# Kernel optimization log

Hardware: AMD Instinct MI355X
Metric: run time of the kernel (lower is better)

## Reference

```python
import jax, jax.numpy as jnp
import numpy as np

N_NODES = 100000
N_EDGES = 1600000
D_FEAT = 64  # node feature dim; apply_func indim = 2*D_FEAT, outdim = D_FEAT


def setup_inputs() -> dict:
    key = jax.random.key(0)
    k1, k2, k3, k4 = jax.random.split(key, 4)
    h = jax.random.normal(k1, (N_NODES, D_FEAT), dtype=jnp.float32)
    src = jax.random.randint(k2, (N_EDGES,), 0, N_NODES, dtype=jnp.int32)
    dst = jax.random.randint(k3, (N_EDGES,), 0, N_NODES, dtype=jnp.int32)
    W = jax.random.normal(k4, (D_FEAT, 2 * D_FEAT), dtype=jnp.float32) / jnp.sqrt(2.0 * D_FEAT)
    b = jnp.zeros((D_FEAT,), dtype=jnp.float32)
    return {"h": h, "W": W, "b": b, "src": src, "dst": dst}


def reference(h, W, b, src, dst):
    n = h.shape[0]
    # message passing: gather source features, mean-reduce per destination node
    msgs = h[src]                                                # [E, D]
    summed = jax.ops.segment_sum(msgs, dst, num_segments=n)     # [N, D]
    deg = jax.ops.segment_sum(jnp.ones(dst.shape, h.dtype), dst, num_segments=n)  # [N]
    c = summed / jnp.maximum(deg, 1.0)[:, None]                 # mean aggregate
    # update: concat(h, c) -> linear -> L2 normalize -> relu
    bundle = jnp.concatenate([h, c], axis=1) @ W.T + b           # [N, D]
    norm = jnp.linalg.norm(bundle, axis=1, keepdims=True)
    bundle = bundle / jnp.maximum(norm, 1e-12)                   # F.normalize(p=2, dim=1)
    new_h = jax.nn.relu(bundle)
    # DGL update_all only touches nodes that received messages
    h_upd = jnp.where(deg[:, None] > 0, new_h, h)
    # residual (indim == outdim)
    return h + h_upd
```

## Files before the change

kernel.cpp:

```cpp
#include <hip/hip_runtime.h>

#define DF 64
#define ELLK 32
#define NB 512
#define BSTR 3584
#define NPB 196
#define NSL 4

typedef __attribute__((ext_vector_type(8))) short bf16x8;
typedef __attribute__((ext_vector_type(4))) float f32x4;

__device__ __forceinline__ unsigned short bf16rne(float f) {
    unsigned u = __float_as_uint(f);
    unsigned r = u + 0x7fffu + ((u >> 16) & 1u);
    return (unsigned short)(r >> 16);
}
__device__ __forceinline__ float b2f(unsigned short u) {
    return __uint_as_float((unsigned)u << 16);
}

__global__ __launch_bounds__(256) void conv_zero(
    const float* __restrict__ h, unsigned short* __restrict__ hbs,
    int* __restrict__ gcur, int* __restrict__ ovfcnt, int N)
{
    int tid = blockIdx.x * 256 + threadIdx.x;
    if (tid < NB) gcur[tid] = 0;
    if (tid == NB) *ovfcnt = 0;
    if (tid < N * 8) {
        int n = tid >> 3, s8 = tid & 7;
        const float* hp = &h[(size_t)n * DF + s8 * 8];
        float4 v0 = *(const float4*)hp;
        float4 v1 = *(const float4*)(hp + 4);
        ushort4 o0, o1;
        o0.x = bf16rne(v0.x); o0.y = bf16rne(v0.y); o0.z = bf16rne(v0.z); o0.w = bf16rne(v0.w);
        o1.x = bf16rne(v1.x); o1.y = bf16rne(v1.y); o1.z = bf16rne(v1.z); o1.w = bf16rne(v1.w);
        unsigned short* op = &hbs[((size_t)(s8 >> 1) * (N + 1) + n) * 16 + (s8 & 1) * 8];
        *(ushort4*)op = o0;
        *(ushort4*)(op + 4) = o1;
    }
}

#define EPT 13
__global__ __launch_bounds__(256) void bin_edges(
    const int* __restrict__ src, const int* __restrict__ dst,
    int* __restrict__ gcur, unsigned* __restrict__ pairs,
    int* __restrict__ ovf, int* __restrict__ ovfcnt, int ovfcap, int E, int N)
{
    __shared__ unsigned hist[NB];
    __shared__ unsigned base_s[NB];
    int t = threadIdx.x;
    for (int i = t; i < NB; i += 256) hist[i] = 0;
    __syncthreads();

    int e0 = blockIdx.x * (EPT * 256);
    unsigned pk[EPT];
    #pragma unroll
    for (int k = 0; k < EPT; ++k) {
        int e = e0 + k * 256 + t;
        pk[k] = 0xFFFFFFFFu;
        if (e < E) {
            int d = dst[e];
            unsigned bkt = (unsigned)(((unsigned long long)d * NB) / (unsigned)N);
            unsigned r = atomicAdd(&hist[bkt], 1u);
            pk[k] = (r << 9) | bkt;
        }
    }
    __syncthreads();
    int rot = (blockIdx.x * 67) & (NB - 1);
    for (int i = t; i < NB; i += 256) {
        int ii = (i + rot) & (NB - 1);
        unsigned hv = hist[ii];
        if (hv) base_s[ii] = (unsigned)atomicAdd(&gcur[ii], (int)hv);
    }
    __syncthreads();

    #pragma unroll
    for (int k = 0; k < EPT; ++k) {
        if (pk[k] != 0xFFFFFFFFu) {
            int e = e0 + k * 256 + t;
            int d = dst[e], s = src[e];
            unsigned bkt = pk[k] & (NB - 1u);
            unsigned pos = base_s[bkt] + (pk[k] >> 9);
            if (pos < BSTR) {
                int lo = (int)(((long long)bkt * N + NB - 1) / NB);
                pairs[(size_t)bkt * BSTR + pos] = ((unsigned)(d - lo) << 17) | (unsigned)s;
            } else {
                int p = atomicAdd(ovfcnt, 1);
                if (p < ovfcap) { ovf[2 * p] = d; ovf[2 * p + 1] = s; }
            }
        }
    }
}

__global__ __launch_bounds__(256) void build_ell(
    const unsigned* __restrict__ pairs, const int* __restrict__ gcur,
    int* __restrict__ cnt, int* __restrict__ ell,
    int* __restrict__ ovf, int* __restrict__ ovfcnt, int ovfcap, int N)
{
    __shared__ int ell_l[NPB * ELLK];
    __shared__ int cnt_l[NPB];
    int b = blockIdx.x, t = threadIdx.x;
    int lo = (int)(((long long)b * N + NB - 1) / NB);
    int hi = (int)(((long long)(b + 1) * N + NB - 1) / NB);
    if (hi > N) hi = N;
    int nn = hi - lo;
    for (int i = t; i < nn; i += 256) cnt_l[i] = 0;
    __syncthreads();

    int count = gcur[b]; if (count > BSTR) count = BSTR;
    const unsigned* pb = &pairs[(size_t)b * BSTR];
    for (int i = t; i < count; i += 256) {
        unsigned p = pb[i];
        int ld = (int)(p >> 17);
        int s  = (int)(p & 131071u);
        int slot = atomicAdd(&cnt_l[ld], 1);
        if (slot < ELLK) {
            ell_l[ld * ELLK + (((slot & 7) << 2) | (slot >> 3))] = s;
        } else {
            int q = atomicAdd(ovfcnt, 1);
            if (q < ovfcap) { ovf[2 * q] = lo + ld; ovf[2 * q + 1] = s; }
        }
    }
    __syncthreads();

    int total = nn * ELLK;
    int* eout = &ell[(size_t)lo * ELLK];
    for (int i = t; i < total; i += 256) eout[i] = ell_l[i];
    for (int i = t; i < nn; i += 256) {
        int c = cnt_l[i];
        cnt[lo + i] = c < ELLK ? c : ELLK;
    }
}

__global__ __launch_bounds__(512) void gather_slice(
    const unsigned short* __restrict__ hbs, const int* __restrict__ cnt,
    const int* __restrict__ ell, unsigned short* __restrict__ csum, int N)
{
    int slice = blockIdx.x & 3;
    int wave = threadIdx.x >> 6, lane = threadIdx.x & 63;
    const int ns = lane >> 4;
    const int q  = lane & 15;
    const int nb = q >> 1;
    const int fp = q & 1;
    const unsigned short* tab = hbs + (size_t)slice * (N + 1) * 16;
    unsigned short* cs = csum + (size_t)slice * N * 16;

    int gw = (blockIdx.x >> 2) * 8 + wave;
    int nw = (gridDim.x >> 2) * 8;

    for (int n0 = gw * 4; n0 < N; n0 += nw * 4) {
        int n = n0 + ns;
        bool valid = (n < N);
        int m = valid ? cnt[n] : 0;
        const int* erow = &ell[(size_t)(valid ? n : 0) * ELLK];
        int4 pv = *(const int4*)(erow + nb * 4);

        bf16x8 v0 = {0,0,0,0,0,0,0,0};
        bf16x8 v1 = {0,0,0,0,0,0,0,0};
        bf16x8 v2 = {0,0,0,0,0,0,0,0};
        bf16x8 v3 = {0,0,0,0,0,0,0,0};
        if (nb      < m) v0 = *(const bf16x8*)&tab[(size_t)pv.x * 16 + fp * 8];
        if (nb +  8 < m) v1 = *(const bf16x8*)&tab[(size_t)pv.y * 16 + fp * 8];
        if (nb + 16 < m) v2 = *(const bf16x8*)&tab[(size_t)pv.z * 16 + fp * 8];
        if (nb + 24 < m) v3 = *(const bf16x8*)&tab[(size_t)pv.w * 16 + fp * 8];

        f32x4 lo, hi;
        #pragma unroll
        for (int i = 0; i < 4; ++i) {
            lo[i] = (b2f((unsigned short)v0[i])     + b2f((unsigned short)v1[i]))
                  + (b2f((unsigned short)v2[i])     + b2f((unsigned short)v3[i]));
            hi[i] = (b2f((unsigned short)v0[4 + i]) + b2f((unsigned short)v1[4 + i]))
                  + (b2f((unsigned short)v2[4 + i]) + b2f((unsigned short)v3[4 + i]));
        }

        #pragma unroll
        for (int msk = 2; msk <= 8; msk <<= 1) {
            #pragma unroll
            for (int i = 0; i < 4; ++i) {
                lo[i] += __shfl_xor(lo[i], msk);
                hi[i] += __shfl_xor(hi[i], msk);
            }
        }

        if (valid && nb == 0) {
            bf16x8 o;
            o[0] = (short)bf16rne(lo[0]); o[1] = (short)bf16rne(lo[1]);
            o[2] = (short)bf16rne(lo[2]); o[3] = (short)bf16rne(lo[3]);
            o[4] = (short)bf16rne(hi[0]); o[5] = (short)bf16rne(hi[1]);
            o[6] = (short)bf16rne(hi[2]); o[7] = (short)bf16rne(hi[3]);
            *(bf16x8*)&cs[(size_t)n * 16 + fp * 8] = o;
        }
    }
}

__global__ __launch_bounds__(256) void sage_update_mfma(
    const float* __restrict__ h, const float* __restrict__ W,
    const float* __restrict__ b, const int* __restrict__ cnt,
    const unsigned short* __restrict__ hbs,
    const unsigned short* __restrict__ csum,
    const int* __restrict__ ovf, const int* __restrict__ ovfcnt,
    int ovfcap, float* __restrict__ out, int N)
{
    const int lane = threadIdx.x & 63;
    const int wave = threadIdx.x >> 6;
    const int c = lane & 15;
    const int q = lane >> 4;

    bf16x8 bf[4][4];
    #pragma unroll
    for (int nt = 0; nt < 4; ++nt) {
        #pragma unroll
        for (int kt = 0; kt < 4; ++kt) {
            const float* wp = &W[(size_t)(nt * 16 + c) * 128 + kt * 32 + q * 8];
            float4 w0 = *(const float4*)wp;
            float4 w1 = *(const float4*)(wp + 4);
            bf16x8 f;
            f[0] = (short)bf16rne(w0.x); f[1] = (short)bf16rne(w0.y);
            f[2] = (short)bf16rne(w0.z); f[3] = (short)bf16rne(w0.w);
            f[4] = (short)bf16rne(w1.x); f[5] = (short)bf16rne(w1.y);
            f[6] = (short)bf16rne(w1.z); f[7] = (short)bf16rne(w1.w);
            bf[nt][kt] = f;
        }
    }
    float bias[4];
    #pragma unroll
    for (int nt = 0; nt < 4; ++nt) bias[nt] = b[nt * 16 + c];

    int oc = *ovfcnt; if (oc > ovfcap) oc = ovfcap;

    int gwave = blockIdx.x * 4 + wave;
    int nwave = gridDim.x * 4;
    int ntiles = (N + 15) >> 4;
    const int sl0 = q >> 1;
    const int hf  = (q & 1) * 8;

    for (int tile = gwave; tile < ntiles; tile += nwave) {
        int n0 = tile << 4;
        int nm = n0 + c;
        int nmc = nm < N ? nm : N - 1;
        int deg = cnt[nmc];
        int extra = 0;
        if (oc > 0) {
            for (int t = 0; t < oc; ++t)
                if (ovf[2 * t] == nm) extra++;
        }
        int dtot = deg + extra;
        float inv = 1.0f / fmaxf((float)dtot, 1.0f);

        bf16x8 a0 = *(const bf16x8*)&hbs[((size_t)sl0 * (N + 1) + nmc) * 16 + hf];
        bf16x8 a1 = *(const bf16x8*)&hbs[((size_t)(sl0 + 2) * (N + 1) + nmc) * 16 + hf];
        bf16x8 a2, a3;
        #pragma unroll
        for (int kc = 0; kc < 2; ++kc) {
            int sl = kc * 2 + sl0;
            bf16x8 u = *(const bf16x8*)&csum[((size_t)sl * N + nmc) * 16 + hf];
            float e[8];
            #pragma unroll
            for (int i = 0; i < 8; ++i) e[i] = b2f((unsigned short)u[i]);
            if (oc > 0) {
                for (int t = 0; t < oc; ++t) {
                    if (ovf[2 * t] == nm) {
                        bf16x8 hu = *(const bf16x8*)&hbs[((size_t)sl * (N + 1) + ovf[2 * t + 1]) * 16 + hf];
                        #pragma unroll
                        for (int i = 0; i < 8; ++i) e[i] += b2f((unsigned short)hu[i]);
                    }
                }
            }
            bf16x8 f;
            #pragma unroll
            for (int i = 0; i < 8; ++i) f[i] = (short)bf16rne(e[i] * inv);
            if (kc == 0) a2 = f; else a3 = f;
        }

        f32x4 acc0 = {bias[0], bias[0], bias[0], bias[0]};
        f32x4 acc1 = {bias[1], bias[1], bias[1], bias[1]};
        f32x4 acc2 = {bias[2], bias[2], bias[2], bias[2]};
        f32x4 acc3 = {bias[3], bias[3], bias[3], bias[3]};
        acc0 = __builtin_amdgcn_mfma_f32_16x16x32_bf16(a0, bf[0][0], acc0, 0, 0, 0);
        acc0 = __builtin_amdgcn_mfma_f32_16x16x32_bf16(a1, bf[0][1], acc0, 0, 0, 0);
        acc0 = __builtin_amdgcn_mfma_f32_16x16x32_bf16(a2, bf[0][2], acc0, 0, 0, 0);
        acc0 = __builtin_amdgcn_mfma_f32_16x16x32_bf16(a3, bf[0][3], acc0, 0, 0, 0);
        acc1 = __builtin_amdgcn_mfma_f32_16x16x32_bf16(a0, bf[1][0], acc1, 0, 0, 0);
        acc1 = __builtin_amdgcn_mfma_f32_16x16x32_bf16(a1, bf[1][1], acc1, 0, 0, 0);
        acc1 = __builtin_amdgcn_mfma_f32_16x16x32_bf16(a2, bf[1][2], acc1, 0, 0, 0);
        acc1 = __builtin_amdgcn_mfma_f32_16x16x32_bf16(a3, bf[1][3], acc1, 0, 0, 0);
        acc2 = __builtin_amdgcn_mfma_f32_16x16x32_bf16(a0, bf[2][0], acc2, 0, 0, 0);
        acc2 = __builtin_amdgcn_mfma_f32_16x16x32_bf16(a1, bf[2][1], acc2, 0, 0, 0);
        acc2 = __builtin_amdgcn_mfma_f32_16x16x32_bf16(a2, bf[2][2], acc2, 0, 0, 0);
        acc2 = __builtin_amdgcn_mfma_f32_16x16x32_bf16(a3, bf[2][3], acc2, 0, 0, 0);
        acc3 = __builtin_amdgcn_mfma_f32_16x16x32_bf16(a0, bf[3][0], acc3, 0, 0, 0);
        acc3 = __builtin_amdgcn_mfma_f32_16x16x32_bf16(a1, bf[3][1], acc3, 0, 0, 0);
        acc3 = __builtin_amdgcn_mfma_f32_16x16x32_bf16(a2, bf[3][2], acc3, 0, 0, 0);
        acc3 = __builtin_amdgcn_mfma_f32_16x16x32_bf16(a3, bf[3][3], acc3, 0, 0, 0);

        float ss[4];
        #pragma unroll
        for (int r = 0; r < 4; ++r)
            ss[r] = acc0[r] * acc0[r] + acc1[r] * acc1[r]
                  + acc2[r] * acc2[r] + acc3[r] * acc3[r];
        #pragma unroll
        for (int msk = 1; msk <= 8; msk <<= 1) {
            ss[0] += __shfl_xor(ss[0], msk);
            ss[1] += __shfl_xor(ss[1], msk);
            ss[2] += __shfl_xor(ss[2], msk);
            ss[3] += __shfl_xor(ss[3], msk);
        }
        #pragma unroll
        for (int r = 0; r < 4; ++r) {
            int nr = n0 + q * 4 + r;
            int dr = __shfl(deg + extra, q * 4 + r);
            if (nr < N) {
                float rin = 1.0f / fmaxf(sqrtf(ss[r]), 1e-12f);
                const float* hp = &h[(size_t)nr * DF + c];
                float hv0 = hp[0], hv1 = hp[16], hv2 = hp[32], hv3 = hp[48];
                bool up = dr > 0;
                float o0 = hv0 + (up ? fmaxf(acc0[r] * rin, 0.f) : hv0);
                float o1 = hv1 + (up ? fmaxf(acc1[r] * rin, 0.f) : hv1);
                float o2 = hv2 + (up ? fmaxf(acc2[r] * rin, 0.f) : hv2);
                float o3 = hv3 + (up ? fmaxf(acc3[r] * rin, 0.f) : hv3);
                float* op = &out[(size_t)nr * DF + c];
                op[0] = o0; op[16] = o1; op[32] = o2; op[48] = o3;
            }
        }
    }
}

extern "C" void kernel_launch(void* const* d_in, const int* in_sizes, int n_in,
                              void* d_out, int out_size, void* d_ws, size_t ws_size,
                              hipStream_t stream) {
    const float* h   = (const float*)d_in[0];
    const float* W   = (const float*)d_in[1];
    const float* b   = (const float*)d_in[2];
    const int*   src = (const int*)d_in[3];
    const int*   dst = (const int*)d_in[4];
    float* out = (float*)d_out;

    const int N = in_sizes[0] / DF;
    const int E = in_sizes[3];

    int* cnt    = (int*)d_ws;
    int* ovfcnt = cnt + N;
    int* gcur   = cnt + ((N + 31) & ~15);
    int* ell    = gcur + ((NB + 15) & ~15);
    unsigned short* hbs  = (unsigned short*)(ell + (((size_t)N * ELLK + 15) & ~(size_t)15));
    unsigned short* csum = hbs + (((size_t)(N + 1) * DF + 15) & ~(size_t)15);
    unsigned* pairs = (unsigned*)(csum + (((size_t)N * DF + 15) & ~(size_t)15));
    int* ovf    = (int*)(pairs + (size_t)NB * BSTR);
    size_t used = (size_t)((char*)ovf - (char*)d_ws);
    int ovfcap  = (ws_size > used + 64) ? (int)((ws_size - used) / 8 - 4) : 0;

    conv_zero<<<(N * 8 + 255) / 256, 256, 0, stream>>>(h, hbs, gcur, ovfcnt, N);

    bin_edges<<<(E + EPT * 256 - 1) / (EPT * 256), 256, 0, stream>>>(
        src, dst, gcur, pairs, ovf, ovfcnt, ovfcap, E, N);

    build_ell<<<NB, 256, 0, stream>>>(pairs, gcur, cnt, ell, ovf, ovfcnt, ovfcap, N);

    gather_slice<<<2048, 512, 0, stream>>>(hbs, cnt, ell, csum, N);

    sage_update_mfma<<<512, 256, 0, stream>>>(
        h, W, b, cnt, hbs, csum, ovf, ovfcnt, ovfcap, out, N);
}
```

Measured before the change: 202.8 us.

## Fuse ELL build and gather into per-bucket LDS atomic accumulation

Replaces the build_ell plus gather_slice pair with one kernel per destination bucket. Each block walks its binned edge pairs, gathers bf16 source rows, and accumulates them into an fp32 LDS tile using shared atomics, then writes bf16 sums and degrees. This drops the ELL intermediate, its cap of 32 neighbours per node, and one kernel launch, and switches the feature table to a plain row-major layout. The cost is heavy LDS float atomic traffic and, with twice as many buckets, half the per-bucket capacity, so more edges may overflow into the slow overflow path.

```diff
diff --git a/kernel.cpp b/kernel.cpp
--- a/kernel.cpp
+++ b/kernel.cpp
@@ -1,11 +1,10 @@
 #include <hip/hip_runtime.h>
 
 #define DF 64
-#define ELLK 32
-#define NB 512
-#define BSTR 3584
-#define NPB 196
-#define NSL 4
+#define NB 1024
+#define BSTR 1792
+#define NPB 98
+#define APAD 65
 
 typedef __attribute__((ext_vector_type(8))) short bf16x8;
 typedef __attribute__((ext_vector_type(4))) float f32x4;
@@ -27,14 +26,14 @@
     if (tid < NB) gcur[tid] = 0;
     if (tid == NB) *ovfcnt = 0;
     if (tid < N * 8) {
-        int n = tid >> 3, s8 = tid & 7;
-        const float* hp = &h[(size_t)n * DF + s8 * 8];
+        int n = tid >> 3, f8 = tid & 7;
+        const float* hp = &h[(size_t)n * DF + f8 * 8];
         float4 v0 = *(const float4*)hp;
         float4 v1 = *(const float4*)(hp + 4);
         ushort4 o0, o1;
         o0.x = bf16rne(v0.x); o0.y = bf16rne(v0.y); o0.z = bf16rne(v0.z); o0.w = bf16rne(v0.w);
         o1.x = bf16rne(v1.x); o1.y = bf16rne(v1.y); o1.z = bf16rne(v1.z); o1.w = bf16rne(v1.w);
-        unsigned short* op = &hbs[((size_t)(s8 >> 1) * (N + 1) + n) * 16 + (s8 & 1) * 8];
+        unsigned short* op = &hbs[(size_t)n * DF + f8 * 8];
         *(ushort4*)op = o0;
         *(ushort4*)(op + 4) = o1;
     }
@@ -62,7 +61,7 @@
             int d = dst[e];
             unsigned bkt = (unsigned)(((unsigned long long)d * NB) / (unsigned)N);
             unsigned r = atomicAdd(&hist[bkt], 1u);
-            pk[k] = (r << 9) | bkt;
+            pk[k] = (r << 10) | bkt;
         }
     }
     __syncthreads();
@@ -80,7 +79,7 @@
             int e = e0 + k * 256 + t;
             int d = dst[e], s = src[e];
             unsigned bkt = pk[k] & (NB - 1u);
-            unsigned pos = base_s[bkt] + (pk[k] >> 9);
+            unsigned pos = base_s[bkt] + (pk[k] >> 10);
             if (pos < BSTR) {
                 int lo = (int)(((long long)bkt * N + NB - 1) / NB);
                 pairs[(size_t)bkt * BSTR + pos] = ((unsigned)(d - lo) << 17) | (unsigned)s;
@@ -92,105 +91,54 @@
     }
 }
 
-__global__ __launch_bounds__(256) void build_ell(
+__global__ __launch_bounds__(512) void gather_bucket(
     const unsigned* __restrict__ pairs, const int* __restrict__ gcur,
-    int* __restrict__ cnt, int* __restrict__ ell,
-    int* __restrict__ ovf, int* __restrict__ ovfcnt, int ovfcap, int N)
+    const unsigned short* __restrict__ hbs,
+    int* __restrict__ cnt, unsigned short* __restrict__ csum, int N)
 {
-    __shared__ int ell_l[NPB * ELLK];
+    __shared__ float acc[NPB * APAD];
     __shared__ int cnt_l[NPB];
     int b = blockIdx.x, t = threadIdx.x;
     int lo = (int)(((long long)b * N + NB - 1) / NB);
     int hi = (int)(((long long)(b + 1) * N + NB - 1) / NB);
     if (hi > N) hi = N;
     int nn = hi - lo;
-    for (int i = t; i < nn; i += 256) cnt_l[i] = 0;
+
+    for (int i = t; i < nn * APAD; i += 512) acc[i] = 0.f;
+    for (int i = t; i < nn; i += 512) cnt_l[i] = 0;
     __syncthreads();
 
     int count = gcur[b]; if (count > BSTR) count = BSTR;
     const unsigned* pb = &pairs[(size_t)b * BSTR];
-    for (int i = t; i < count; i += 256) {
-        unsigned p = pb[i];
-        int ld = (int)(p >> 17);
-        int s  = (int)(p & 131071u);
-        int slot = atomicAdd(&cnt_l[ld], 1);
-        if (slot < ELLK) {
-            ell_l[ld * ELLK + (((slot & 7) << 2) | (slot >> 3))] = s;
-        } else {
-            int q = atomicAdd(ovfcnt, 1);
-            if (q < ovfcap) { ovf[2 * q] = lo + ld; ovf[2 * q + 1] = s; }
-        }
-    }
-    __syncthreads();
-
-    int total = nn * ELLK;
-    int* eout = &ell[(size_t)lo * ELLK];
-    for (int i = t; i < total; i += 256) eout[i] = ell_l[i];
-    for (int i = t; i < nn; i += 256) {
-        int c = cnt_l[i];
-        cnt[lo + i] = c < ELLK ? c : ELLK;
-    }
-}
-
-__global__ __launch_bounds__(512) void gather_slice(
-    const unsigned short* __restrict__ hbs, const int* __restrict__ cnt,
-    const int* __restrict__ ell, unsigned short* __restrict__ csum, int N)
-{
-    int slice = blockIdx.x & 3;
-    int wave = threadIdx.x >> 6, lane = threadIdx.x & 63;
-    const int ns = lane >> 4;
-    const int q  = lane & 15;
-    const int nb = q >> 1;
-    const int fp = q & 1;
-    const unsigned short* tab = hbs + (size_t)slice * (N + 1) * 16;
-    unsigned short* cs = csum + (size_t)slice * N * 16;
-
-    int gw = (blockIdx.x >> 2) * 8 + wave;
-    int nw = (gridDim.x >> 2) * 8;
-
-    for (int n0 = gw * 4; n0 < N; n0 += nw * 4) {
-        int n = n0 + ns;
-        bool valid = (n < N);
-        int m = valid ? cnt[n] : 0;
-        const int* erow = &ell[(size_t)(valid ? n : 0) * ELLK];
-        int4 pv = *(const int4*)(erow + nb * 4);
-
-        bf16x8 v0 = {0,0,0,0,0,0,0,0};
-        bf16x8 v1 = {0,0,0,0,0,0,0,0};
-        bf16x8 v2 = {0,0,0,0,0,0,0,0};
-        bf16x8 v3 = {0,0,0,0,0,0,0,0};
-        if (nb      < m) v0 = *(const bf16x8*)&tab[(size_t)pv.x * 16 + fp * 8];
-        if (nb +  8 < m) v1 = *(const bf16x8*)&tab[(size_t)pv.y * 16 + fp * 8];
-        if (nb + 16 < m) v2 = *(const bf16x8*)&tab[(size_t)pv.z * 16 + fp * 8];
-        if (nb + 24 < m) v3 = *(const bf16x8*)&tab[(size_t)pv.w * 16 + fp * 8];
-
-        f32x4 lo, hi;
-        #pragma unroll
-        for (int i = 0; i < 4; ++i) {
-            lo[i] = (b2f((unsigned short)v0[i])     + b2f((unsigned short)v1[i]))
-                  + (b2f((unsigned short)v2[i])     + b2f((unsigned short)v3[i]));
-            hi[i] = (b2f((unsigned short)v0[4 + i]) + b2f((unsigned short)v1[4 + i]))
-                  + (b2f((unsigned short)v2[4 + i]) + b2f((unsigned short)v3[4 + i]));
-        }
-
-        #pragma unroll
-        for (int msk = 2; msk <= 8; msk <<= 1) {
+    const int lane = t & 63, wv = t >> 6;
+    const int ew = lane >> 3;
+    const int f8 = lane & 7;
+
+    for (int i0 = wv * 8; i0 < count; i0 += 64) {
+        int e = i0 + ew;
+        if (e < count) {
+            unsigned p = pb[e];
+            int ld = (int)(p >> 17);
+            int s  = (int)(p & 131071u);
+            bf16x8 u = *(const bf16x8*)&hbs[(size_t)s * DF + f8 * 8];
+            if (f8 == 0) atomicAdd(&cnt_l[ld], 1);
+            float* ap = &acc[ld * APAD + f8 * 8];
             #pragma unroll
-            for (int i = 0; i < 4; ++i) {
-                lo[i] += __shfl_xor(lo[i], msk);
-                hi[i] += __shfl_xor(hi[i], msk);
-            }
-        }
-
-        if (valid && nb == 0) {
-            bf16x8 o;
-            o[0] = (short)bf16rne(lo[0]); o[1] = (short)bf16rne(lo[1]);
-            o[2] = (short)bf16rne(lo[2]); o[3] = (short)bf16rne(lo[3]);
-            o[4] = (short)bf16rne(hi[0]); o[5] = (short)bf16rne(hi[1]);
-            o[6] = (short)bf16rne(hi[2]); o[7] = (short)bf16rne(hi[3]);
-            *(bf16x8*)&cs[(size_t)n * 16 + fp * 8] = o;
-        }
-    }
+            for (int j = 0; j < 8; ++j)
+                atomicAdd(&ap[j], b2f((unsigned short)u[j]));
+        }
+    }
+    __syncthreads();
+
+    for (int i = t; i < nn * 8; i += 512) {
+        int node = i >> 3, fb = (i & 7) * 8;
+        const float* ap = &acc[node * APAD + fb];
+        bf16x8 o;
+        #pragma unroll
+        for (int j = 0; j < 8; ++j) o[j] = (short)bf16rne(ap[j]);
+        *(bf16x8*)&csum[(size_t)(lo + node) * DF + fb] = o;
+    }
+    for (int i = t; i < nn; i += 512) cnt[lo + i] = cnt_l[i];
 }
 
 __global__ __launch_bounds__(256) void sage_update_mfma(
@@ -231,8 +179,6 @@
     int gwave = blockIdx.x * 4 + wave;
     int nwave = gridDim.x * 4;
     int ntiles = (N + 15) >> 4;
-    const int sl0 = q >> 1;
-    const int hf  = (q & 1) * 8;
 
     for (int tile = gwave; tile < ntiles; tile += nwave) {
         int n0 = tile << 4;
@@ -247,20 +193,19 @@
         int dtot = deg + extra;
         float inv = 1.0f / fmaxf((float)dtot, 1.0f);
 
-        bf16x8 a0 = *(const bf16x8*)&hbs[((size_t)sl0 * (N + 1) + nmc) * 16 + hf];
-        bf16x8 a1 = *(const bf16x8*)&hbs[((size_t)(sl0 + 2) * (N + 1) + nmc) * 16 + hf];
+        bf16x8 a0 = *(const bf16x8*)&hbs[(size_t)nmc * DF + q * 8];
+        bf16x8 a1 = *(const bf16x8*)&hbs[(size_t)nmc * DF + 32 + q * 8];
         bf16x8 a2, a3;
         #pragma unroll
         for (int kc = 0; kc < 2; ++kc) {
-            int sl = kc * 2 + sl0;
-            bf16x8 u = *(const bf16x8*)&csum[((size_t)sl * N + nmc) * 16 + hf];
+            bf16x8 u = *(const bf16x8*)&csum[(size_t)nmc * DF + kc * 32 + q * 8];
             float e[8];
             #pragma unroll
             for (int i = 0; i < 8; ++i) e[i] = b2f((unsigned short)u[i]);
             if (oc > 0) {
                 for (int t = 0; t < oc; ++t) {
                     if (ovf[2 * t] == nm) {
-                        bf16x8 hu = *(const bf16x8*)&hbs[((size_t)sl * (N + 1) + ovf[2 * t + 1]) * 16 + hf];
+                        bf16x8 hu = *(const bf16x8*)&hbs[(size_t)ovf[2 * t + 1] * DF + kc * 32 + q * 8];
                         #pragma unroll
                         for (int i = 0; i < 8; ++i) e[i] += b2f((unsigned short)hu[i]);
                     }
@@ -341,9 +286,8 @@
     int* cnt    = (int*)d_ws;
     int* ovfcnt = cnt + N;
     int* gcur   = cnt + ((N + 31) & ~15);
-    int* ell    = gcur + ((NB + 15) & ~15);
-    unsigned short* hbs  = (unsigned short*)(ell + (((size_t)N * ELLK + 15) & ~(size_t)15));
-    unsigned short* csum = hbs + (((size_t)(N + 1) * DF + 15) & ~(size_t)15);
+    unsigned short* hbs  = (unsigned short*)(gcur + ((NB + 15) & ~15));
+    unsigned short* csum = hbs + (((size_t)N * DF + 15) & ~(size_t)15);
     unsigned* pairs = (unsigned*)(csum + (((size_t)N * DF + 15) & ~(size_t)15));
     int* ovf    = (int*)(pairs + (size_t)NB * BSTR);
     size_t used = (size_t)((char*)ovf - (char*)d_ws);
@@ -354,9 +298,7 @@
     bin_edges<<<(E + EPT * 256 - 1) / (EPT * 256), 256, 0, stream>>>(
         src, dst, gcur, pairs, ovf, ovfcnt, ovfcap, E, N);
 
-    build_ell<<<NB, 256, 0, stream>>>(pairs, gcur, cnt, ell, ovf, ovfcnt, ovfcap, N);
-
-    gather_slice<<<2048, 512, 0, stream>>>(hbs, cnt, ell, csum, N);
+    gather_bucket<<<NB, 512, 0, stream>>>(pairs, gcur, hbs, cnt, csum, N);
 
     sage_update_mfma<<<512, 256, 0, stream>>>(
         h, W, b, cnt, hbs, csum, ovf, ovfcnt, ovfcap, out, N);
```

After: 669.0 us. 3.3x slower.
